# Kernel tuning notes

Hardware: AMD Instinct MI355X
Metric: run time of the kernel (lower is better)

The kernel has to match this reference:

```python
import jax, jax.numpy as jnp
import numpy as np

B, S, D, H, T_OUT = 256, 256, 64, 1024, 32  # batch, enc seq, input dim, hidden, decode steps


def setup_inputs() -> dict:
    key = jax.random.key(0)
    ks = jax.random.split(key, 15)
    p = lambda k, shape: jax.random.normal(k, shape, jnp.float32) * 0.05
    return {
        "X": jax.random.normal(ks[0], (B, S, D), jnp.float32),
        # encoder LSTM (2 layers); bias = b_ih + b_hh fused (same math)
        "enc_Wih0": p(ks[1], (4 * H, D)), "enc_Whh0": p(ks[2], (4 * H, H)), "enc_b0": p(ks[3], (4 * H,)),
        "enc_Wih1": p(ks[4], (4 * H, H)), "enc_Whh1": p(ks[5], (4 * H, H)), "enc_b1": p(ks[6], (4 * H,)),
        # decoder LSTM (2 layers, scalar input)
        "dec_Wih0": p(ks[7], (4 * H, 1)), "dec_Whh0": p(ks[8], (4 * H, H)), "dec_b0": p(ks[9], (4 * H,)),
        "dec_Wih1": p(ks[10], (4 * H, H)), "dec_Whh1": p(ks[11], (4 * H, H)), "dec_b1": p(ks[12], (4 * H,)),
        # output projection hidden -> 1
        "fc_W": p(ks[13], (1, H)), "fc_b": p(ks[14], (1,)),
    }


def _cell(x, h, c, Wih, Whh, b):
    # torch LSTM cell, gate order i, f, g, o
    gates = x @ Wih.T + h @ Whh.T + b  # [B, 4H]
    i, f, g, o = jnp.split(gates, 4, axis=-1)
    c = jax.nn.sigmoid(f) * c + jax.nn.sigmoid(i) * jnp.tanh(g)
    h = jax.nn.sigmoid(o) * jnp.tanh(c)
    return h, c


def reference(X, enc_Wih0, enc_Whh0, enc_b0, enc_Wih1, enc_Whh1, enc_b1,
              dec_Wih0, dec_Whh0, dec_b0, dec_Wih1, dec_Whh1, dec_b1,
              fc_W, fc_b):
    batch = X.shape[0]
    zeros = jnp.zeros((batch, H), X.dtype)

    def enc_layer(Wih, Whh, b, xs):  # xs: [S, B, Din]
        def step(carry, x_t):
            h, c = carry
            h, c = _cell(x_t, h, c, Wih, Whh, b)
            return (h, c), h
        (h, c), hs = jax.lax.scan(step, (zeros, zeros), xs)
        return hs, h, c

    xs = jnp.swapaxes(X, 0, 1)  # time-major [S, B, D]
    hs0, h0, c0 = enc_layer(enc_Wih0, enc_Whh0, enc_b0, xs)
    _, h1, c1 = enc_layer(enc_Wih1, enc_Whh1, enc_b1, hs0)

    inp0 = jnp.zeros((batch, 1), X.dtype)

    def dec_step(carry, _):
        dh0, dc0, dh1, dc1, inp = carry
        dh0, dc0 = _cell(inp, dh0, dc0, dec_Wih0, dec_Whh0, dec_b0)
        dh1, dc1 = _cell(dh0, dh1, dc1, dec_Wih1, dec_Whh1, dec_b1)
        pred = dh1 @ fc_W.T + fc_b  # [B, 1]; dropout is identity at inference
        return (dh0, dc0, dh1, dc1, pred), pred

    _, preds = jax.lax.scan(dec_step, (h0, c0, h1, c1, inp0), None, length=T_OUT)
    return jnp.transpose(preds, (1, 0, 2))  # [B, T_OUT, 1]
```

## Files before the change

kernel.cpp:

```cpp
#include <hip/hip_runtime.h>

#define B_ 256
#define S_ 256
#define D_ 64
#define H_ 1024
#define G4 4096
#define TOUT 32

typedef unsigned short u16;
typedef __attribute__((ext_vector_type(8))) short short8;
typedef __attribute__((ext_vector_type(4))) float float4v;

__device__ __forceinline__ float bf2f(u16 b) {
  return __uint_as_float(((unsigned int)b) << 16);
}
__device__ __forceinline__ u16 f2bf(float f) {
  unsigned int u = __float_as_uint(f);
  unsigned int r = (u + 0x7fffu + ((u >> 16) & 1u)) >> 16;
  return (u16)r;
}
__device__ __forceinline__ unsigned pack2(float a, float b) {
  return (unsigned)f2bf(a) | ((unsigned)f2bf(b) << 16);
}
__device__ __forceinline__ float sigm(float x) {
  return 1.f / (1.f + __expf(-x));
}
__device__ __forceinline__ float tanh_(float x) {
  float xc = fminf(fmaxf(x, -15.f), 15.f);
  float e = __expf(2.f * xc);
  return (e - 1.f) / (e + 1.f);
}

__global__ __launch_bounds__(256) void cvt_kernel(const float* __restrict__ src,
                                                  u16* __restrict__ dst, int n) {
  for (int i = blockIdx.x * blockDim.x + threadIdx.x; i < n;
       i += gridDim.x * blockDim.x)
    dst[i] = f2bf(src[i]);
}

__global__ __launch_bounds__(256) void zero_kernel(uint4* __restrict__ p, int n16) {
  for (int i = blockIdx.x * blockDim.x + threadIdx.x; i < n16;
       i += gridDim.x * blockDim.x)
    p[i] = make_uint4(0u, 0u, 0u, 0u);
}

struct LayerDesc {
  const u16* A0; int lda0;
  const u16* A1; int lda1; int klen0;
  const void* W0; int ldw0;
  const void* W1; int ldw1; int Ktot;
  const float* bias;
  const float* wcol;
  const float* inp;
  float* c;
  u16* h;
  int active;
};

template <bool WF32>
__global__ __launch_bounds__(256) void lstm_step_kernel(LayerDesc dA, LayerDesc dB)
{
  const bool second = (blockIdx.y >= 4);
  const LayerDesc d = second ? dB : dA;
  if (!d.active) return;

  __shared__ u16 As[64][72];
  __shared__ u16 Bs[64][72];
  __shared__ float Gs[64][68];

  const int tid = threadIdx.x;
  const int m0 = (second ? (blockIdx.y - 4) : blockIdx.y) * 64;
  const int n0 = blockIdx.x * 64;
  const int ub = n0 >> 2;
  const int r = tid >> 2;
  const int q = tid & 3;
  const int lane = tid & 63;
  const int wv = tid >> 6;
  const int wm = (wv >> 1) * 32;
  const int wn = (wv & 1) * 32;
  const int l16 = lane & 15;
  const int quad = lane >> 4;

  const int klen0 = d.klen0;
  const u16* aw0 = d.A0 + (size_t)(m0 + r) * d.lda0;
  const u16* aw1 = d.A1 + (size_t)(m0 + r) * d.lda1;
  const int orow = (r & 3) * H_ + ub + (r >> 2);
  const u16* bw0_h = (const u16*)d.W0 + (size_t)orow * d.ldw0;
  const u16* bw1_h = (const u16*)d.W1 + (size_t)orow * d.ldw1;
  const float* bw0_f = (const float*)d.W0 + (size_t)orow * d.ldw0;
  const float* bw1_f = (const float*)d.W1 + (size_t)orow * d.ldw1;

  uint4 av0, av1, bv0, bv1;
  float4 bf0, bf1, bf2, bf3;

  auto load_chunk = [&](int kc) {
    const int kg = kc * 64 + q * 16;
    const bool first = kg < klen0;
    const u16* pa = first ? (aw0 + kg) : (aw1 + (kg - klen0));
    av0 = *(const uint4*)pa;
    av1 = *(const uint4*)(pa + 8);
    if constexpr (WF32) {
      const float* pb = first ? (bw0_f + kg) : (bw1_f + (kg - klen0));
      bf0 = *(const float4*)pb;
      bf1 = *(const float4*)(pb + 4);
      bf2 = *(const float4*)(pb + 8);
      bf3 = *(const float4*)(pb + 12);
    } else {
      const u16* pb = first ? (bw0_h + kg) : (bw1_h + (kg - klen0));
      bv0 = *(const uint4*)pb;
      bv1 = *(const uint4*)(pb + 8);
    }
  };

  float4v acc00 = {}, acc01 = {}, acc10 = {}, acc11 = {};
  const int nch = d.Ktot >> 6;
  load_chunk(0);
  for (int kc = 0; kc < nch; ++kc) {
    if constexpr (WF32) {
      bv0 = make_uint4(pack2(bf0.x, bf0.y), pack2(bf0.z, bf0.w),
                       pack2(bf1.x, bf1.y), pack2(bf1.z, bf1.w));
      bv1 = make_uint4(pack2(bf2.x, bf2.y), pack2(bf2.z, bf2.w),
                       pack2(bf3.x, bf3.y), pack2(bf3.z, bf3.w));
    }
    __syncthreads();
    *(uint4*)&As[r][q * 16]     = av0;
    *(uint4*)&As[r][q * 16 + 8] = av1;
    *(uint4*)&Bs[r][q * 16]     = bv0;
    *(uint4*)&Bs[r][q * 16 + 8] = bv1;
    __syncthreads();
    if (kc + 1 < nch) load_chunk(kc + 1);
#pragma unroll
    for (int ks = 0; ks < 2; ++ks) {
      const int kb = ks * 32 + quad * 8;
      short8 a0 = *(const short8*)&As[wm + l16][kb];
      short8 a1 = *(const short8*)&As[wm + 16 + l16][kb];
      short8 b0 = *(const short8*)&Bs[wn + l16][kb];
      short8 b1 = *(const short8*)&Bs[wn + 16 + l16][kb];
      acc00 = __builtin_amdgcn_mfma_f32_16x16x32_bf16(a0, b0, acc00, 0, 0, 0);
      acc01 = __builtin_amdgcn_mfma_f32_16x16x32_bf16(a0, b1, acc01, 0, 0, 0);
      acc10 = __builtin_amdgcn_mfma_f32_16x16x32_bf16(a1, b0, acc10, 0, 0, 0);
      acc11 = __builtin_amdgcn_mfma_f32_16x16x32_bf16(a1, b1, acc11, 0, 0, 0);
    }
  }

#pragma unroll
  for (int rr = 0; rr < 4; ++rr) {
    Gs[wm + quad * 4 + rr][wn + l16]           = acc00[rr];
    Gs[wm + quad * 4 + rr][wn + 16 + l16]      = acc01[rr];
    Gs[wm + 16 + quad * 4 + rr][wn + l16]      = acc10[rr];
    Gs[wm + 16 + quad * 4 + rr][wn + 16 + l16] = acc11[rr];
  }
  __syncthreads();

#pragma unroll
  for (int it = 0; it < 4; ++it) {
    const int p = tid + it * 256;
    const int bl = p >> 4;
    const int u = p & 15;
    const int J = ub + u;
    const int bg = m0 + bl;
    const float4v g = *(const float4v*)&Gs[bl][u * 4];
    float pi = g[0] + d.bias[J];
    float pf = g[1] + d.bias[H_ + J];
    float pg = g[2] + d.bias[2 * H_ + J];
    float po = g[3] + d.bias[3 * H_ + J];
    if (d.inp != nullptr) {
      const float iv = d.inp[bg];
      pi += iv * d.wcol[J];
      pf += iv * d.wcol[H_ + J];
      pg += iv * d.wcol[2 * H_ + J];
      po += iv * d.wcol[3 * H_ + J];
    }
    const size_t idx = (size_t)bg * H_ + J;
    const float c = d.c[idx];
    const float cn = sigm(pf) * c + sigm(pi) * tanh_(pg);
    d.c[idx] = cn;
    d.h[idx] = f2bf(sigm(po) * tanh_(cn));
  }
}

__global__ __launch_bounds__(256) void fc_kernel(
    const u16* __restrict__ h1, const float* __restrict__ fcW,
    const float* __restrict__ fcb, float* __restrict__ out,
    float* __restrict__ inp, int t)
{
  const int b = blockIdx.x;
  const int tid = threadIdx.x;
  const u16* hr = h1 + (size_t)b * H_ + tid * 4;
  const float* wr = fcW + tid * 4;
  float s = 0.f;
#pragma unroll
  for (int j = 0; j < 4; ++j) s += bf2f(hr[j]) * wr[j];
#pragma unroll
  for (int off = 32; off > 0; off >>= 1) s += __shfl_down(s, off, 64);
  __shared__ float red[4];
  if ((tid & 63) == 0) red[tid >> 6] = s;
  __syncthreads();
  if (tid == 0) {
    const float p = red[0] + red[1] + red[2] + red[3] + fcb[0];
    out[(size_t)b * TOUT + t] = p;
    inp[b] = p;
  }
}

extern "C" void kernel_launch(void* const* d_in, const int* in_sizes, int n_in,
                              void* d_out, int out_size, void* d_ws, size_t ws_size,
                              hipStream_t stream)
{
  const float* X     = (const float*)d_in[0];
  const float* eWih0 = (const float*)d_in[1];
  const float* eWhh0 = (const float*)d_in[2];
  const float* eb0   = (const float*)d_in[3];
  const float* eWih1 = (const float*)d_in[4];
  const float* eWhh1 = (const float*)d_in[5];
  const float* eb1   = (const float*)d_in[6];
  const float* dWih0 = (const float*)d_in[7];
  const float* dWhh0 = (const float*)d_in[8];
  const float* db0   = (const float*)d_in[9];
  const float* dWih1 = (const float*)d_in[10];
  const float* dWhh1 = (const float*)d_in[11];
  const float* db1   = (const float*)d_in[12];
  const float* fcW   = (const float*)d_in[13];
  const float* fcb   = (const float*)d_in[14];
  float* out = (float*)d_out;

  char* ws = (char*)d_ws;
  size_t off = 0;
  auto alloc = [&](size_t bytes) -> void* {
    void* p = ws + off;
    off += (bytes + 255) & ~(size_t)255;
    return p;
  };
  u16* h0buf[2], *h1buf[2];
  h0buf[0] = (u16*)alloc((size_t)B_ * H_ * 2);
  h0buf[1] = (u16*)alloc((size_t)B_ * H_ * 2);
  h1buf[0] = (u16*)alloc((size_t)B_ * H_ * 2);
  h1buf[1] = (u16*)alloc((size_t)B_ * H_ * 2);
  float* C0  = (float*)alloc((size_t)B_ * H_ * 4);
  float* C1  = (float*)alloc((size_t)B_ * H_ * 4);
  float* INP = (float*)alloc(B_ * 4);
  const size_t zbytes = off;
  u16* XB = (u16*)alloc((size_t)B_ * S_ * D_ * 2);
  u16* WB_eWih0 = (u16*)alloc((size_t)G4 * D_ * 2);
  u16* WB_eWhh0 = (u16*)alloc((size_t)G4 * H_ * 2);
  u16* WB_eWih1 = (u16*)alloc((size_t)G4 * H_ * 2);
  u16* WB_eWhh1 = (u16*)alloc((size_t)G4 * H_ * 2);
  u16* WB_dWhh0 = (u16*)alloc((size_t)G4 * H_ * 2);
  u16* WB_dWih1 = (u16*)alloc((size_t)G4 * H_ * 2);
  u16* WB_dWhh1 = (u16*)alloc((size_t)G4 * H_ * 2);
  const size_t need_full = off;
  const bool fast = (ws_size >= need_full);

  zero_kernel<<<dim3(256), dim3(256), 0, stream>>>((uint4*)ws, (int)(zbytes / 16));
  cvt_kernel<<<dim3(1024), dim3(256), 0, stream>>>(X, XB, B_ * S_ * D_);
  if (fast) {
    cvt_kernel<<<dim3(256), dim3(256), 0, stream>>>(eWih0, WB_eWih0, G4 * D_);
    cvt_kernel<<<dim3(1024), dim3(256), 0, stream>>>(eWhh0, WB_eWhh0, G4 * H_);
    cvt_kernel<<<dim3(1024), dim3(256), 0, stream>>>(eWih1, WB_eWih1, G4 * H_);
    cvt_kernel<<<dim3(1024), dim3(256), 0, stream>>>(eWhh1, WB_eWhh1, G4 * H_);
    cvt_kernel<<<dim3(1024), dim3(256), 0, stream>>>(dWhh0, WB_dWhh0, G4 * H_);
    cvt_kernel<<<dim3(1024), dim3(256), 0, stream>>>(dWih1, WB_dWih1, G4 * H_);
    cvt_kernel<<<dim3(1024), dim3(256), 0, stream>>>(dWhh1, WB_dWhh1, G4 * H_);
  }

  auto mk = [&](const u16* A0, int lda0, const u16* A1, int lda1, int klen0,
                const void* W0b, const void* W0f, int ldw0,
                const void* W1b, const void* W1f, int ldw1, int Ktot,
                const float* bias, const float* wcol, const float* inp,
                float* c, u16* h) {
    LayerDesc d;
    d.A0 = A0; d.lda0 = lda0; d.A1 = A1; d.lda1 = lda1; d.klen0 = klen0;
    d.W0 = fast ? W0b : W0f; d.ldw0 = ldw0;
    d.W1 = fast ? W1b : W1f; d.ldw1 = ldw1; d.Ktot = Ktot;
    d.bias = bias; d.wcol = wcol; d.inp = inp; d.c = c; d.h = h;
    d.active = 1;
    return d;
  };
  LayerDesc off_d = {};
  off_d.active = 0;

  auto launch = [&](dim3 grid, const LayerDesc& a, const LayerDesc& b) {
    if (fast)
      lstm_step_kernel<false><<<grid, dim3(256), 0, stream>>>(a, b);
    else
      lstm_step_kernel<true><<<grid, dim3(256), 0, stream>>>(a, b);
  };

  for (int u = 0; u <= S_; ++u) {
    LayerDesc d0 = off_d, d1 = off_d;
    if (u < S_) {
      const int t = u;
      d0 = mk(XB + t * D_, S_ * D_, h0buf[t & 1], H_, D_,
              WB_eWih0, eWih0, D_, WB_eWhh0, eWhh0, H_, 1088,
              eb0, nullptr, nullptr, C0, h0buf[(t + 1) & 1]);
    }
    if (u >= 1) {
      const int t = u - 1;
      d1 = mk(h0buf[(t + 1) & 1], H_, h1buf[t & 1], H_, H_,
              WB_eWih1, eWih1, H_, WB_eWhh1, eWhh1, H_, 2048,
              eb1, nullptr, nullptr, C1, h1buf[(t + 1) & 1]);
    }
    launch(dim3(64, 8), d0, d1);
  }

  for (int t = 0; t < TOUT; ++t) {
    u16* h0i = h0buf[t & 1]; u16* h0o = h0buf[(t + 1) & 1];
    u16* h1i = h1buf[t & 1]; u16* h1o = h1buf[(t + 1) & 1];
    LayerDesc dl0 = mk(h0i, H_, h0i, H_, 1024,
                       WB_dWhh0, dWhh0, H_, WB_dWhh0, dWhh0, H_, 1024,
                       db0, dWih0, INP, C0, h0o);
    launch(dim3(64, 4), dl0, off_d);
    LayerDesc dl1 = mk(h0o, H_, h1i, H_, H_,
                       WB_dWih1, dWih1, H_, WB_dWhh1, dWhh1, H_, 2048,
                       db1, nullptr, nullptr, C1, h1o);
    launch(dim3(64, 4), dl1, off_d);
    fc_kernel<<<dim3(B_), dim3(256), 0, stream>>>(h1o, fcW, fcb, out, INP, t);
  }
}
```

Baseline: 7.247 ms.

## Stream weights via global_load_lds double buffer and load A fragments directly

Reworks the LSTM step GEMM main loop. The bf16 weight tile is fetched with global_load_lds straight into a double-buffered LDS array laid out in MFMA fragment order. The activation operand is read from global memory directly into registers in MFMA layout, so it no longer goes through LDS. Together these drop one of the two barriers per K chunk and the register-to-LDS staging copies, and let the next chunk's loads overlap the current MFMAs. In exchange, two waves now load the same A rows redundantly, and the loop depends on the barrier also waiting for the asynchronous LDS loads to land.

```diff
diff --git a/kernel.cpp b/kernel.cpp
--- a/kernel.cpp
+++ b/kernel.cpp
@@ -29,6 +29,12 @@
   float xc = fminf(fmaxf(x, -15.f), 15.f);
   float e = __expf(2.f * xc);
   return (e - 1.f) / (e + 1.f);
+}
+
+__device__ __forceinline__ void gload_lds16(const void* g, void* l) {
+  __builtin_amdgcn_global_load_lds(
+      (const __attribute__((address_space(1))) void*)g,
+      (__attribute__((address_space(3))) void*)l, 16, 0, 0);
 }
 
 __global__ __launch_bounds__(256) void cvt_kernel(const float* __restrict__ src,
@@ -64,82 +70,110 @@
   const LayerDesc d = second ? dB : dA;
   if (!d.active) return;
 
-  __shared__ u16 As[64][72];
-  __shared__ u16 Bs[64][72];
+  __shared__ __align__(16) u16 BsF[2][8][64][8];
   __shared__ float Gs[64][68];
 
   const int tid = threadIdx.x;
   const int m0 = (second ? (blockIdx.y - 4) : blockIdx.y) * 64;
   const int n0 = blockIdx.x * 64;
   const int ub = n0 >> 2;
-  const int r = tid >> 2;
-  const int q = tid & 3;
   const int lane = tid & 63;
   const int wv = tid >> 6;
   const int wm = (wv >> 1) * 32;
   const int wn = (wv & 1) * 32;
   const int l16 = lane & 15;
   const int quad = lane >> 4;
-
   const int klen0 = d.klen0;
-  const u16* aw0 = d.A0 + (size_t)(m0 + r) * d.lda0;
-  const u16* aw1 = d.A1 + (size_t)(m0 + r) * d.lda1;
-  const int orow = (r & 3) * H_ + ub + (r >> 2);
-  const u16* bw0_h = (const u16*)d.W0 + (size_t)orow * d.ldw0;
-  const u16* bw1_h = (const u16*)d.W1 + (size_t)orow * d.ldw1;
-  const float* bw0_f = (const float*)d.W0 + (size_t)orow * d.ldw0;
-  const float* bw1_f = (const float*)d.W1 + (size_t)orow * d.ldw1;
-
-  uint4 av0, av1, bv0, bv1;
-  float4 bf0, bf1, bf2, bf3;
-
-  auto load_chunk = [&](int kc) {
-    const int kg = kc * 64 + q * 16;
-    const bool first = kg < klen0;
-    const u16* pa = first ? (aw0 + kg) : (aw1 + (kg - klen0));
-    av0 = *(const uint4*)pa;
-    av1 = *(const uint4*)(pa + 8);
+
+  const int c0 = (wv >> 1) * 16 + l16;
+  const int kloc = (wv & 1) * 32 + quad * 8;
+  const int orow = (c0 & 3) * H_ + ub + (c0 >> 2);
+  const u16* w0h0 = (const u16*)d.W0 + (size_t)orow * d.ldw0;
+  const u16* w0h1 = w0h0 + (size_t)8 * d.ldw0;
+  const u16* w1h0 = (const u16*)d.W1 + (size_t)orow * d.ldw1;
+  const u16* w1h1 = w1h0 + (size_t)8 * d.ldw1;
+  const float* f0h0 = (const float*)d.W0 + (size_t)orow * d.ldw0;
+  const float* f0h1 = f0h0 + (size_t)8 * d.ldw0;
+  const float* f1h0 = (const float*)d.W1 + (size_t)orow * d.ldw1;
+  const float* f1h1 = f1h0 + (size_t)8 * d.ldw1;
+
+  const int ar0 = m0 + wm + l16;
+  const u16* a00 = d.A0 + (size_t)ar0 * d.lda0;
+  const u16* a01 = d.A0 + (size_t)(ar0 + 16) * d.lda0;
+  const u16* a10 = d.A1 + (size_t)ar0 * d.lda1;
+  const u16* a11 = d.A1 + (size_t)(ar0 + 16) * d.lda1;
+  const int akoff = quad * 8;
+
+  float4 fB[4];
+
+  auto loadBf = [&](int kc) {
+    const int k = kc * 64 + kloc;
+    const bool first = k < klen0;
+    const int kk = first ? k : k - klen0;
+    const float* p0 = (first ? f0h0 : f1h0) + kk;
+    const float* p1 = (first ? f0h1 : f1h1) + kk;
+    fB[0] = *(const float4*)p0;
+    fB[1] = *(const float4*)(p0 + 4);
+    fB[2] = *(const float4*)p1;
+    fB[3] = *(const float4*)(p1 + 4);
+  };
+
+  auto issue_dma = [&](int kc, int buf) {
+    const int k = kc * 64 + kloc;
+    const bool first = k < klen0;
+    const int kk = first ? k : k - klen0;
+    gload_lds16((first ? w0h0 : w1h0) + kk, &BsF[buf][wv][0][0]);
+    gload_lds16((first ? w0h1 : w1h1) + kk, &BsF[buf][wv + 4][0][0]);
+  };
+
+  auto loadA = [&](int kc, short8* ar) {
+#pragma unroll
+    for (int ks = 0; ks < 2; ++ks) {
+      const int k = kc * 64 + ks * 32 + akoff;
+      const bool first = k < klen0;
+      const int kk = first ? k : k - klen0;
+      ar[ks]     = *(const short8*)((first ? a00 : a10) + kk);
+      ar[2 + ks] = *(const short8*)((first ? a01 : a11) + kk);
+    }
+  };
+
+  float4v acc00 = {}, acc01 = {}, acc10 = {}, acc11 = {};
+  short8 aA[4], aN[4];
+  const int nch = d.Ktot >> 6;
+
+  loadA(0, aA);
+  if constexpr (WF32) loadBf(0);
+  else issue_dma(0, 0);
+
+  for (int kc = 0; kc < nch; ++kc) {
+    const int buf = kc & 1;
     if constexpr (WF32) {
-      const float* pb = first ? (bw0_f + kg) : (bw1_f + (kg - klen0));
-      bf0 = *(const float4*)pb;
-      bf1 = *(const float4*)(pb + 4);
-      bf2 = *(const float4*)(pb + 8);
-      bf3 = *(const float4*)(pb + 12);
-    } else {
-      const u16* pb = first ? (bw0_h + kg) : (bw1_h + (kg - klen0));
-      bv0 = *(const uint4*)pb;
-      bv1 = *(const uint4*)(pb + 8);
-    }
-  };
-
-  float4v acc00 = {}, acc01 = {}, acc10 = {}, acc11 = {};
-  const int nch = d.Ktot >> 6;
-  load_chunk(0);
-  for (int kc = 0; kc < nch; ++kc) {
-    if constexpr (WF32) {
-      bv0 = make_uint4(pack2(bf0.x, bf0.y), pack2(bf0.z, bf0.w),
-                       pack2(bf1.x, bf1.y), pack2(bf1.z, bf1.w));
-      bv1 = make_uint4(pack2(bf2.x, bf2.y), pack2(bf2.z, bf2.w),
-                       pack2(bf3.x, bf3.y), pack2(bf3.z, bf3.w));
+      uint4 bW0 = make_uint4(pack2(fB[0].x, fB[0].y), pack2(fB[0].z, fB[0].w),
+                             pack2(fB[1].x, fB[1].y), pack2(fB[1].z, fB[1].w));
+      uint4 bW1 = make_uint4(pack2(fB[2].x, fB[2].y), pack2(fB[2].z, fB[2].w),
+                             pack2(fB[3].x, fB[3].y), pack2(fB[3].z, fB[3].w));
+      *(uint4*)&BsF[buf][wv][lane][0]     = bW0;
+      *(uint4*)&BsF[buf][wv + 4][lane][0] = bW1;
     }
     __syncthreads();
-    *(uint4*)&As[r][q * 16]     = av0;
-    *(uint4*)&As[r][q * 16 + 8] = av1;
-    *(uint4*)&Bs[r][q * 16]     = bv0;
-    *(uint4*)&Bs[r][q * 16 + 8] = bv1;
-    __syncthreads();
-    if (kc + 1 < nch) load_chunk(kc + 1);
+    const bool more = (kc + 1 < nch);
+    if (more) {
+      if constexpr (WF32) loadBf(kc + 1);
+      else issue_dma(kc + 1, buf ^ 1);
+      loadA(kc + 1, aN);
+    }
 #pragma unroll
     for (int ks = 0; ks < 2; ++ks) {
-      const int kb = ks * 32 + quad * 8;
-      short8 a0 = *(const short8*)&As[wm + l16][kb];
-      short8 a1 = *(const short8*)&As[wm + 16 + l16][kb];
-      short8 b0 = *(const short8*)&Bs[wn + l16][kb];
-      short8 b1 = *(const short8*)&Bs[wn + 16 + l16][kb];
-      acc00 = __builtin_amdgcn_mfma_f32_16x16x32_bf16(a0, b0, acc00, 0, 0, 0);
-      acc01 = __builtin_amdgcn_mfma_f32_16x16x32_bf16(a0, b1, acc01, 0, 0, 0);
-      acc10 = __builtin_amdgcn_mfma_f32_16x16x32_bf16(a1, b0, acc10, 0, 0, 0);
-      acc11 = __builtin_amdgcn_mfma_f32_16x16x32_bf16(a1, b1, acc11, 0, 0, 0);
+      const short8 b0 = *(const short8*)&BsF[buf][(wn >> 3) + ks][lane][0];
+      const short8 b1 = *(const short8*)&BsF[buf][(wn >> 3) + 2 + ks][lane][0];
+      acc00 = __builtin_amdgcn_mfma_f32_16x16x32_bf16(aA[ks], b0, acc00, 0, 0, 0);
+      acc01 = __builtin_amdgcn_mfma_f32_16x16x32_bf16(aA[ks], b1, acc01, 0, 0, 0);
+      acc10 = __builtin_amdgcn_mfma_f32_16x16x32_bf16(aA[2 + ks], b0, acc10, 0, 0, 0);
+      acc11 = __builtin_amdgcn_mfma_f32_16x16x32_bf16(aA[2 + ks], b1, acc11, 0, 0, 0);
+    }
+    if (more) {
+#pragma unroll
+      for (int i = 0; i < 4; ++i) aA[i] = aN[i];
     }
   }
 
```

Measured after the change: 13.90 ms. +91.8%, slower.

## Split K across waves with private LDS tiles and 32x32 MFMA, reduce via LDS

Applied to the files above, without the earlier changes.

The LSTM step GEMM now gives each of the four waves its own K-chunks (interleaved by 4) and its own LDS staging tile. This removes the block-wide __syncthreads inside the K loop. Each wave computes the full 64x64 tile with 32x32x16 bf16 MFMAs, and the partial sums are then reduced across waves through shared memory before the gate nonlinearity. The trade-offs are more LDS (about 57KB), which may reduce occupancy, 64 accumulator registers per thread, and an extra cross-wave reduction.

```diff
diff --git a/kernel.cpp b/kernel.cpp
--- a/kernel.cpp
+++ b/kernel.cpp
@@ -10,6 +10,7 @@
 typedef unsigned short u16;
 typedef __attribute__((ext_vector_type(8))) short short8;
 typedef __attribute__((ext_vector_type(4))) float float4v;
+typedef __attribute__((ext_vector_type(16))) float f32x16;
 
 __device__ __forceinline__ float bf2f(u16 b) {
   return __uint_as_float(((unsigned int)b) << 16);
@@ -64,91 +65,131 @@
   const LayerDesc d = second ? dB : dA;
   if (!d.active) return;
 
-  __shared__ u16 As[64][72];
-  __shared__ u16 Bs[64][72];
-  __shared__ float Gs[64][68];
+  __shared__ __align__(16) unsigned char SMEM[58368];
 
   const int tid = threadIdx.x;
+  const int lane = tid & 63;
+  const int wv = tid >> 6;
+  u16* As_w = (u16*)(SMEM + wv * 10240);
+  u16* Bs_w = (u16*)(SMEM + wv * 10240 + 5120);
+  float* Gs = (float*)(SMEM + 40960);
+
   const int m0 = (second ? (blockIdx.y - 4) : blockIdx.y) * 64;
   const int n0 = blockIdx.x * 64;
   const int ub = n0 >> 2;
-  const int r = tid >> 2;
-  const int q = tid & 3;
-  const int lane = tid & 63;
-  const int wv = tid >> 6;
-  const int wm = (wv >> 1) * 32;
-  const int wn = (wv & 1) * 32;
-  const int l16 = lane & 15;
-  const int quad = lane >> 4;
-
   const int klen0 = d.klen0;
-  const u16* aw0 = d.A0 + (size_t)(m0 + r) * d.lda0;
-  const u16* aw1 = d.A1 + (size_t)(m0 + r) * d.lda1;
-  const int orow = (r & 3) * H_ + ub + (r >> 2);
-  const u16* bw0_h = (const u16*)d.W0 + (size_t)orow * d.ldw0;
-  const u16* bw1_h = (const u16*)d.W1 + (size_t)orow * d.ldw1;
-  const float* bw0_f = (const float*)d.W0 + (size_t)orow * d.ldw0;
-  const float* bw1_f = (const float*)d.W1 + (size_t)orow * d.ldw1;
-
-  uint4 av0, av1, bv0, bv1;
-  float4 bf0, bf1, bf2, bf3;
-
-  auto load_chunk = [&](int kc) {
-    const int kg = kc * 64 + q * 16;
+
+  const u16* gA0 = d.A0 + (size_t)(m0 + lane) * d.lda0;
+  const u16* gA1 = d.A1 + (size_t)(m0 + lane) * d.lda1;
+  const int orow = (lane & 3) * H_ + ub + (lane >> 2);
+  const u16* gB0h = (const u16*)d.W0 + (size_t)orow * d.ldw0;
+  const u16* gB1h = (const u16*)d.W1 + (size_t)orow * d.ldw1;
+  const float* gB0f = (const float*)d.W0 + (size_t)orow * d.ldw0;
+  const float* gB1f = (const float*)d.W1 + (size_t)orow * d.ldw1;
+
+  uint4 rA[4], rB[4];
+  float4 rBf[8];
+
+  auto loadG = [&](int c) {
+    const int kg = c * 32;
     const bool first = kg < klen0;
-    const u16* pa = first ? (aw0 + kg) : (aw1 + (kg - klen0));
-    av0 = *(const uint4*)pa;
-    av1 = *(const uint4*)(pa + 8);
+    const int kk = first ? kg : kg - klen0;
+    const uint4* pa = (const uint4*)((first ? gA0 : gA1) + kk);
+    rA[0] = pa[0]; rA[1] = pa[1]; rA[2] = pa[2]; rA[3] = pa[3];
     if constexpr (WF32) {
-      const float* pb = first ? (bw0_f + kg) : (bw1_f + (kg - klen0));
-      bf0 = *(const float4*)pb;
-      bf1 = *(const float4*)(pb + 4);
-      bf2 = *(const float4*)(pb + 8);
-      bf3 = *(const float4*)(pb + 12);
+      const float4* pb = (const float4*)((first ? gB0f : gB1f) + kk);
+#pragma unroll
+      for (int j = 0; j < 8; ++j) rBf[j] = pb[j];
     } else {
-      const u16* pb = first ? (bw0_h + kg) : (bw1_h + (kg - klen0));
-      bv0 = *(const uint4*)pb;
-      bv1 = *(const uint4*)(pb + 8);
-    }
-  };
-
-  float4v acc00 = {}, acc01 = {}, acc10 = {}, acc11 = {};
-  const int nch = d.Ktot >> 6;
-  load_chunk(0);
-  for (int kc = 0; kc < nch; ++kc) {
+      const uint4* pb = (const uint4*)((first ? gB0h : gB1h) + kk);
+      rB[0] = pb[0]; rB[1] = pb[1]; rB[2] = pb[2]; rB[3] = pb[3];
+    }
+  };
+
+  auto writeL = [&]() {
     if constexpr (WF32) {
-      bv0 = make_uint4(pack2(bf0.x, bf0.y), pack2(bf0.z, bf0.w),
-                       pack2(bf1.x, bf1.y), pack2(bf1.z, bf1.w));
-      bv1 = make_uint4(pack2(bf2.x, bf2.y), pack2(bf2.z, bf2.w),
-                       pack2(bf3.x, bf3.y), pack2(bf3.z, bf3.w));
-    }
-    __syncthreads();
-    *(uint4*)&As[r][q * 16]     = av0;
-    *(uint4*)&As[r][q * 16 + 8] = av1;
-    *(uint4*)&Bs[r][q * 16]     = bv0;
-    *(uint4*)&Bs[r][q * 16 + 8] = bv1;
-    __syncthreads();
-    if (kc + 1 < nch) load_chunk(kc + 1);
-#pragma unroll
-    for (int ks = 0; ks < 2; ++ks) {
-      const int kb = ks * 32 + quad * 8;
-      short8 a0 = *(const short8*)&As[wm + l16][kb];
-      short8 a1 = *(const short8*)&As[wm + 16 + l16][kb];
-      short8 b0 = *(const short8*)&Bs[wn + l16][kb];
-      short8 b1 = *(const short8*)&Bs[wn + 16 + l16][kb];
-      acc00 = __builtin_amdgcn_mfma_f32_16x16x32_bf16(a0, b0, acc00, 0, 0, 0);
-      acc01 = __builtin_amdgcn_mfma_f32_16x16x32_bf16(a0, b1, acc01, 0, 0, 0);
-      acc10 = __builtin_amdgcn_mfma_f32_16x16x32_bf16(a1, b0, acc10, 0, 0, 0);
-      acc11 = __builtin_amdgcn_mfma_f32_16x16x32_bf16(a1, b1, acc11, 0, 0, 0);
-    }
-  }
-
-#pragma unroll
-  for (int rr = 0; rr < 4; ++rr) {
-    Gs[wm + quad * 4 + rr][wn + l16]           = acc00[rr];
-    Gs[wm + quad * 4 + rr][wn + 16 + l16]      = acc01[rr];
-    Gs[wm + 16 + quad * 4 + rr][wn + l16]      = acc10[rr];
-    Gs[wm + 16 + quad * 4 + rr][wn + 16 + l16] = acc11[rr];
+#pragma unroll
+      for (int j = 0; j < 4; ++j)
+        rB[j] = make_uint4(pack2(rBf[2 * j].x, rBf[2 * j].y),
+                           pack2(rBf[2 * j].z, rBf[2 * j].w),
+                           pack2(rBf[2 * j + 1].x, rBf[2 * j + 1].y),
+                           pack2(rBf[2 * j + 1].z, rBf[2 * j + 1].w));
+    }
+#pragma unroll
+    for (int j = 0; j < 4; ++j) {
+      *(uint4*)&As_w[lane * 40 + j * 8] = rA[j];
+      *(uint4*)&Bs_w[lane * 40 + j * 8] = rB[j];
+    }
+  };
+
+  f32x16 acc00 = {}, acc01 = {}, acc10 = {}, acc11 = {};
+  const int l31 = lane & 31;
+  const int kh = (lane >> 5) * 8;
+  const int nch = d.Ktot >> 5;
+
+  int c = wv;
+  loadG(c);
+  writeL();
+  if (c + 4 < nch) loadG(c + 4);
+  for (; c < nch; c += 4) {
+#pragma unroll
+    for (int s = 0; s < 2; ++s) {
+      const int ko = s * 16 + kh;
+      const short8 a0 = *(const short8*)&As_w[l31 * 40 + ko];
+      const short8 a1 = *(const short8*)&As_w[(l31 + 32) * 40 + ko];
+      const short8 b0 = *(const short8*)&Bs_w[l31 * 40 + ko];
+      const short8 b1 = *(const short8*)&Bs_w[(l31 + 32) * 40 + ko];
+      acc00 = __builtin_amdgcn_mfma_f32_32x32x16_bf16(a0, b0, acc00, 0, 0, 0);
+      acc01 = __builtin_amdgcn_mfma_f32_32x32x16_bf16(a0, b1, acc01, 0, 0, 0);
+      acc10 = __builtin_amdgcn_mfma_f32_32x32x16_bf16(a1, b0, acc10, 0, 0, 0);
+      acc11 = __builtin_amdgcn_mfma_f32_32x32x16_bf16(a1, b1, acc11, 0, 0, 0);
+    }
+    if (c + 4 < nch) {
+      writeL();
+      if (c + 8 < nch) loadG(c + 8);
+    }
+  }
+
+  __syncthreads();
+
+  auto store_frag = [&](const f32x16& A, int q) {
+    if (q == wv) return;
+    const int slot = (wv > q) ? (wv - 1) : wv;
+    float* rg = (float*)SMEM + (q * 3 + slot) * 1024 + lane * 4;
+#pragma unroll
+    for (int j4 = 0; j4 < 4; ++j4)
+      *(float4*)&rg[j4 * 256] = make_float4(A[j4 * 4 + 0], A[j4 * 4 + 1],
+                                            A[j4 * 4 + 2], A[j4 * 4 + 3]);
+  };
+  store_frag(acc00, 0);
+  store_frag(acc01, 1);
+  store_frag(acc10, 2);
+  store_frag(acc11, 3);
+  __syncthreads();
+
+  f32x16 fin = (wv == 0) ? acc00 : (wv == 1) ? acc01 : (wv == 2) ? acc10 : acc11;
+#pragma unroll
+  for (int s = 0; s < 3; ++s) {
+    const float* rg = (const float*)SMEM + (wv * 3 + s) * 1024 + lane * 4;
+#pragma unroll
+    for (int j4 = 0; j4 < 4; ++j4) {
+      const float4 v = *(const float4*)&rg[j4 * 256];
+      fin[j4 * 4 + 0] += v.x;
+      fin[j4 * 4 + 1] += v.y;
+      fin[j4 * 4 + 2] += v.z;
+      fin[j4 * 4 + 3] += v.w;
+    }
+  }
+  __syncthreads();
+
+  {
+    const int rbase = (wv >> 1) * 32 + (lane >> 5) * 4;
+    const int col = (wv & 1) * 32 + l31;
+#pragma unroll
+    for (int j = 0; j < 16; ++j) {
+      const int row = rbase + (j & 3) + 8 * (j >> 2);
+      Gs[row * 68 + col] = fin[j];
+    }
   }
   __syncthreads();
 
@@ -159,7 +200,7 @@
     const int u = p & 15;
     const int J = ub + u;
     const int bg = m0 + bl;
-    const float4v g = *(const float4v*)&Gs[bl][u * 4];
+    const float4v g = *(const float4v*)&Gs[bl * 68 + u * 4];
     float pi = g[0] + d.bias[J];
     float pf = g[1] + d.bias[H_ + J];
     float pg = g[2] + d.bias[2 * H_ + J];
@@ -172,8 +213,8 @@
       po += iv * d.wcol[3 * H_ + J];
     }
     const size_t idx = (size_t)bg * H_ + J;
-    const float c = d.c[idx];
-    const float cn = sigm(pf) * c + sigm(pi) * tanh_(pg);
+    const float c0 = d.c[idx];
+    const float cn = sigm(pf) * c0 + sigm(pi) * tanh_(pg);
     d.c[idx] = cn;
     d.h[idx] = f2bf(sigm(po) * tanh_(cn));
   }
```

Result: slower. 21.65 ms (+198.8%).
